# Kernel optimization log

Measured on AMD Instinct MI355X. Metric: run time of the kernel, lower is better.

## Reference

```python
import jax, jax.numpy as jnp
import numpy as np

NUM_Q = 4096     # num_of_questions
MAX_STEP = 256   # max_step
BATCH = 64       # students per batch


def setup_inputs() -> dict:
    key = jax.random.key(0)
    k1, k2, k3, k4, k5, k6 = jax.random.split(key, 6)
    # simulated interaction sequences with random leading padding (all-zero rows)
    q_ids = jax.random.randint(k1, (BATCH, MAX_STEP), 0, NUM_Q)
    correct = jax.random.bernoulli(k2, 0.6, (BATCH, MAX_STEP)).astype(jnp.float32)
    start = jax.random.randint(k3, (BATCH,), 0, 16)  # leading pad length per student
    valid = (jnp.arange(MAX_STEP)[None, :] >= start[:, None]).astype(jnp.float32)
    oh = jax.nn.one_hot(q_ids, NUM_Q, dtype=jnp.float32)  # [B,S,Q]
    # batch = [one-hot if answered correctly | one-hot if answered incorrectly]
    batch = jnp.concatenate(
        [oh * (correct * valid)[..., None], oh * ((1.0 - correct) * valid)[..., None]],
        axis=-1,
    )  # [B,S,2Q]
    pred = jax.random.uniform(k4, (BATCH, MAX_STEP, NUM_Q), minval=0.01, maxval=0.99)
    target_q = jax.random.uniform(k5, (BATCH, 1), minval=0.01, maxval=0.99)
    target_label = jax.random.bernoulli(k6, 0.5, (BATCH,)).astype(jnp.float32)
    return {"pred": pred, "target_q": target_q, "batch": batch, "target_label": target_label}


def _bce(p, a):
    # elementwise BCE matching torch.nn.BCELoss (log clamped at -100)
    logp = jnp.maximum(jnp.log(p), -100.0)
    log1mp = jnp.maximum(jnp.log1p(-p), -100.0)
    return -(a * logp + (1.0 - a) * log1mp)


def reference(pred, target_q, batch, target_label):
    Q, S = NUM_Q, MAX_STEP
    delta = batch[:, :, :Q] + batch[:, :, Q:]  # [B,S,Q] one-hot of asked question
    # temp.gather(0, arange) extracts the diagonal of pred[:S-1] @ delta[1:].T,
    # i.e. p[s,j] = pred[s,j] . delta[s,j+1]
    p = jnp.einsum('bsq,bsq->bs', pred[:, :S - 1], delta[:, 1:])  # [B,S-1]
    # correctness label: 1 if correct, 0 if incorrect or padded ('//' is non-diff)
    a = jax.lax.stop_gradient(
        jnp.floor(((batch[:, :, :Q] - batch[:, :, Q:]).sum(-1) + 1.0) / 2.0)
    )[:, 1:]  # [B,S-1]
    # the break loop trims everything before the first p[i] > 0;
    # if no p > 0, argmax returns 0 == no trim (matching torch, where break never fires)
    i = jnp.argmax(p > 0, axis=1)  # [B]
    mask = jnp.arange(S - 1)[None, :] >= i[:, None]
    seq_loss = jnp.sum(jnp.where(mask, _bce(p, a), 0.0), axis=1)  # [B]
    tail = _bce(target_q[:, 0], target_label)  # [B]
    # per-student mean over (trimmed length + 1 appended target)
    n = ((S - 1) - i + 1).astype(pred.dtype)
    return jnp.sum((seq_loss + tail) / n)
```

## Files before the change

kernel.cpp:

```cpp
#include <hip/hip_runtime.h>
#include <limits.h>

#define NUM_Q    4096
#define MAX_STEP 256
#define BATCH    64
#define TWOQ     8192
#define ROWS     (BATCH * MAX_STEP)
#define ITERS    32

__global__ void __launch_bounds__(256) find_onehot_kernel(
        const float* __restrict__ batch,
        const float* __restrict__ pred,
        int* __restrict__ qa,
        float* __restrict__ pw,
        float* __restrict__ out, int out_n) {
    const int gtid = blockIdx.x * blockDim.x + threadIdx.x;
    if (gtid < out_n) out[gtid] = 0.0f;

    const int row  = gtid >> 6;
    const int lane = gtid & 63;
    if (row >= ROWS) return;
    const int s = row & (MAX_STEP - 1);
    if (s == 0) return;

    const float4* rp = (const float4*)(batch + (size_t)row * TWOQ);

    int found = -1;
    for (int it = 0; it < ITERS; ++it) {
        const float4 v = rp[it * 64 + lane];
        const float sum = v.x + v.y + v.z + v.w;
        const unsigned long long m = __ballot(sum > 0.0f);
        if (m) {
            const int src = __ffsll(m) - 1;
            int idx = 0;
            if (lane == src) {
                const int base = (it * 64 + lane) * 4;
                idx = (v.x != 0.f) ? base
                    : (v.y != 0.f) ? base + 1
                    : (v.z != 0.f) ? base + 2
                                   : base + 3;
            }
            found = __shfl(idx, src);
            break;
        }
    }

    if (lane == 0) {
        qa[row] = found;
        float p = 0.0f;
        if (found >= 0) {
            const int b   = row >> 8;
            const int qid = found & (NUM_Q - 1);
            p = pred[((size_t)b * MAX_STEP + (s - 1)) * NUM_Q + qid];
        }
        pw[row] = p;
    }
}

__device__ __forceinline__ float bce(float p, float a) {
    float lp  = fmaxf(logf(p), -100.0f);
    float l1p = fmaxf(log1pf(-p), -100.0f);
    return -(a * lp + (1.0f - a) * l1p);
}

__global__ void __launch_bounds__(256) loss_kernel(
        const float* __restrict__ target_q,
        const float* __restrict__ target_label,
        const int* __restrict__ qa,
        const float* __restrict__ pw,
        float* __restrict__ out) {
    const int b    = blockIdx.x;
    const int t    = threadIdx.x;
    const int lane = t & 63;
    const int wid  = t >> 6;
    const int SM1  = MAX_STEP - 1;

    __shared__ int   smin[4];
    __shared__ float ssum[4];

    int   idx = -1;
    float p   = 0.0f;
    if (t < SM1) {
        idx = qa[b * MAX_STEP + t + 1];
        p   = pw[b * MAX_STEP + t + 1];
    }

    int cand = (t < SM1 && p > 0.0f) ? t : INT_MAX;
    #pragma unroll
    for (int off = 32; off > 0; off >>= 1)
        cand = min(cand, __shfl_down(cand, off));
    if (lane == 0) smin[wid] = cand;
    __syncthreads();
    int i0 = min(min(smin[0], smin[1]), min(smin[2], smin[3]));
    if (i0 == INT_MAX) i0 = 0;

    float v = 0.0f;
    if (t < SM1 && t >= i0) {
        const float a = (idx >= 0 && idx < NUM_Q) ? 1.0f : 0.0f;
        v = bce(p, a);
    }
    #pragma unroll
    for (int off = 32; off > 0; off >>= 1)
        v += __shfl_down(v, off);
    if (lane == 0) ssum[wid] = v;
    __syncthreads();

    if (t == 0) {
        const float tail = bce(target_q[b], target_label[b]);
        const float n = (float)(MAX_STEP - i0);
        atomicAdd(out, (ssum[0] + ssum[1] + ssum[2] + ssum[3] + tail) / n);
    }
}

extern "C" void kernel_launch(void* const* d_in, const int* in_sizes, int n_in,
                              void* d_out, int out_size, void* d_ws, size_t ws_size,
                              hipStream_t stream) {
    const float* pred         = (const float*)d_in[0];
    const float* target_q     = (const float*)d_in[1];
    const float* batch        = (const float*)d_in[2];
    const float* target_label = (const float*)d_in[3];
    float* out = (float*)d_out;
    int*   qa  = (int*)d_ws;
    float* pw  = (float*)(qa + ROWS);

    find_onehot_kernel<<<(ROWS * 64) / 256, 256, 0, stream>>>(
        batch, pred, qa, pw, out, out_size);
    loss_kernel<<<BATCH, 256, 0, stream>>>(target_q, target_label, qa, pw, out);
}
```

Baseline: 727.1 us.

## Fuse one-hot search and loss into a single cooperative grid-synced kernel

Merges the one-hot scanning kernel and the per-student loss kernel into one persistent cooperative kernel. Waves loop over rows in grid-stride fashion, alternating row order on odd passes to balance early-exit work, then a grid-wide sync separates the reduction phase. The goal is to remove the second launch and the tail of the first kernel. The cost is a grid barrier, a reduced resident grid, and the assumption that the hard-coded 256 CUs matches the device.

New measurement: 987.7 us. 1.36x slower.

```diff
diff --git a/kernel.cpp b/kernel.cpp
--- a/kernel.cpp
+++ b/kernel.cpp
@@ -1,4 +1,5 @@
 #include <hip/hip_runtime.h>
+#include <hip/hip_cooperative_groups.h>
 #include <limits.h>
 
 #define NUM_Q    4096
@@ -8,54 +9,7 @@
 #define ROWS     (BATCH * MAX_STEP)
 #define ITERS    32
 
-__global__ void __launch_bounds__(256) find_onehot_kernel(
-        const float* __restrict__ batch,
-        const float* __restrict__ pred,
-        int* __restrict__ qa,
-        float* __restrict__ pw,
-        float* __restrict__ out, int out_n) {
-    const int gtid = blockIdx.x * blockDim.x + threadIdx.x;
-    if (gtid < out_n) out[gtid] = 0.0f;
-
-    const int row  = gtid >> 6;
-    const int lane = gtid & 63;
-    if (row >= ROWS) return;
-    const int s = row & (MAX_STEP - 1);
-    if (s == 0) return;
-
-    const float4* rp = (const float4*)(batch + (size_t)row * TWOQ);
-
-    int found = -1;
-    for (int it = 0; it < ITERS; ++it) {
-        const float4 v = rp[it * 64 + lane];
-        const float sum = v.x + v.y + v.z + v.w;
-        const unsigned long long m = __ballot(sum > 0.0f);
-        if (m) {
-            const int src = __ffsll(m) - 1;
-            int idx = 0;
-            if (lane == src) {
-                const int base = (it * 64 + lane) * 4;
-                idx = (v.x != 0.f) ? base
-                    : (v.y != 0.f) ? base + 1
-                    : (v.z != 0.f) ? base + 2
-                                   : base + 3;
-            }
-            found = __shfl(idx, src);
-            break;
-        }
-    }
-
-    if (lane == 0) {
-        qa[row] = found;
-        float p = 0.0f;
-        if (found >= 0) {
-            const int b   = row >> 8;
-            const int qid = found & (NUM_Q - 1);
-            p = pred[((size_t)b * MAX_STEP + (s - 1)) * NUM_Q + qid];
-        }
-        pw[row] = p;
-    }
-}
+namespace cg = cooperative_groups;
 
 __device__ __forceinline__ float bce(float p, float a) {
     float lp  = fmaxf(logf(p), -100.0f);
@@ -63,17 +17,64 @@
     return -(a * lp + (1.0f - a) * l1p);
 }
 
-__global__ void __launch_bounds__(256) loss_kernel(
+__global__ void __launch_bounds__(256) fused_kernel(
+        const float* __restrict__ batch,
+        const float* __restrict__ pred,
         const float* __restrict__ target_q,
         const float* __restrict__ target_label,
-        const int* __restrict__ qa,
-        const float* __restrict__ pw,
+        int* __restrict__ qa,
+        float* __restrict__ pw,
         float* __restrict__ out) {
-    const int b    = blockIdx.x;
-    const int t    = threadIdx.x;
-    const int lane = t & 63;
-    const int wid  = t >> 6;
-    const int SM1  = MAX_STEP - 1;
+    const int t     = threadIdx.x;
+    const int lane  = t & 63;
+    const int gwave = (int)((blockIdx.x * blockDim.x + t) >> 6);
+    const int nwave = (int)((gridDim.x * blockDim.x) >> 6);
+
+    if (blockIdx.x == 0 && t == 0) out[0] = 0.0f;
+
+    for (int base = gwave, pass = 0; base < ROWS; base += nwave, ++pass) {
+        const int row = (pass & 1) ? (base ^ (MAX_STEP - 1)) : base;
+        const int s   = row & (MAX_STEP - 1);
+        if (s == 0) continue;
+
+        const float4* rp = (const float4*)(batch + (size_t)row * TWOQ);
+        int found = -1;
+        for (int it = 0; it < ITERS; ++it) {
+            const float4 v = rp[it * 64 + lane];
+            const float sum = v.x + v.y + v.z + v.w;
+            const unsigned long long m = __ballot(sum > 0.0f);
+            if (m) {
+                const int src = __ffsll(m) - 1;
+                int idx = 0;
+                if (lane == src) {
+                    const int bidx = (it * 64 + lane) * 4;
+                    idx = (v.x != 0.f) ? bidx
+                        : (v.y != 0.f) ? bidx + 1
+                        : (v.z != 0.f) ? bidx + 2
+                                       : bidx + 3;
+                }
+                found = __shfl(idx, src);
+                break;
+            }
+        }
+        if (lane == 0) {
+            qa[row] = found;
+            float p = 0.0f;
+            if (found >= 0) {
+                const int b   = row >> 8;
+                const int qid = found & (NUM_Q - 1);
+                p = pred[((size_t)b * MAX_STEP + (s - 1)) * NUM_Q + qid];
+            }
+            pw[row] = p;
+        }
+    }
+
+    cg::this_grid().sync();
+
+    const int b = blockIdx.x;
+    if (b >= BATCH) return;
+    const int wid = t >> 6;
+    const int SM1 = MAX_STEP - 1;
 
     __shared__ int   smin[4];
     __shared__ float ssum[4];
@@ -123,7 +124,21 @@
     int*   qa  = (int*)d_ws;
     float* pw  = (float*)(qa + ROWS);
 
-    find_onehot_kernel<<<(ROWS * 64) / 256, 256, 0, stream>>>(
-        batch, pred, qa, pw, out, out_size);
-    loss_kernel<<<BATCH, 256, 0, stream>>>(target_q, target_label, qa, pw, out);
+    static int nblk = 0;
+    if (nblk == 0) {
+        int bpc = 0;
+        hipError_t e = hipOccupancyMaxActiveBlocksPerMultiprocessor(
+            &bpc, fused_kernel, 256, 0);
+        if (e != hipSuccess || bpc < 1) bpc = 1;
+        int g = bpc * 256;
+        if (g > ROWS / 4) g = ROWS / 4;
+        g = (g / 64) * 64;
+        if (g < 64) g = 64;
+        nblk = g;
+    }
+
+    void* args[] = { (void*)&batch, (void*)&pred, (void*)&target_q,
+                     (void*)&target_label, (void*)&qa, (void*)&pw, (void*)&out };
+    hipLaunchCooperativeKernel((const void*)fused_kernel, dim3(nblk), dim3(256),
+                               args, 0, stream);
 }
```
